# Kernel optimization log

Measured on AMD Instinct MI355X. Metric: run time of the kernel, lower is better.

Reference implementation:

```python
import jax, jax.numpy as jnp
import numpy as np

B, T, D, E, F, K = 1, 8192, 1024, 8, 4096, 2
CAP_FACTOR = 1.25
AUX_COEFF = 0.01


def setup_inputs() -> dict:
    key = jax.random.key(0)
    k0, k1, k2, k3, k4 = jax.random.split(key, 5)
    x = jax.random.normal(k0, (B, T, D), dtype=jnp.float32)
    Wr = jax.random.normal(k1, (E, D), dtype=jnp.float32) * 0.01  # router, std=0.01 per init
    s = 0.02
    Wg = jax.random.normal(k2, (E, F, D), dtype=jnp.float32) * s  # gate_proj per expert
    Wu = jax.random.normal(k3, (E, F, D), dtype=jnp.float32) * s  # up_proj per expert
    Wd = jax.random.normal(k4, (E, D, F), dtype=jnp.float32) * s  # down_proj per expert
    return {"x": x, "Wr": Wr, "Wg": Wg, "Wu": Wu, "Wd": Wd}


def reference(x, Wr, Wg, Wu, Wd):
    b, t, d = x.shape
    N = b * t
    capacity = max(int(t * K * CAP_FACTOR / E), 1)  # static, matches compute_capacity
    x_flat = x.reshape(N, d)

    # --- router ---
    logits = x_flat @ Wr.T                              # (N, E)
    probs = jax.nn.softmax(logits, axis=-1)
    topw_raw, topi = jax.lax.top_k(probs, K)            # (N, K)
    topw = topw_raw / (topw_raw.sum(-1, keepdims=True) + 1e-9)

    # --- dispatch order: slot-major (slot 0 over all tokens, then slot 1, ...) ---
    flat_e = topi.T.reshape(-1)                         # (K*N,) expert id per assignment
    flat_w = topw.T.reshape(-1)                         # (K*N,)
    tok = jnp.tile(jnp.arange(N), K)                    # (K*N,) token id per assignment

    oh = jax.nn.one_hot(flat_e, E, dtype=jnp.int32)     # (K*N, E)
    rank = (jnp.cumsum(oh, axis=0) - oh)[jnp.arange(K * N), flat_e]  # arrival rank per expert
    accepted = rank < capacity                          # dispatch_mask (slot-major flat)
    pos = jnp.where(accepted, rank, 0)
    dest = flat_e * capacity + pos                      # slot in flattened capacity buffer
    acc_f = accepted.astype(x.dtype)[:, None]

    # scatter tokens into capacity buffers (dropped tokens add zeros)
    buf = jnp.zeros((E * capacity, d), x.dtype).at[dest].add(x_flat[tok] * acc_f)
    expert_in = buf.reshape(E, capacity, d)

    # --- per-expert SwiGLU FFN (batched grouped GEMM) ---
    gate = jax.nn.silu(jnp.einsum('ecd,efd->ecf', expert_in, Wg))
    up = jnp.einsum('ecd,efd->ecf', expert_in, Wu)
    expert_out = jnp.einsum('ecf,edf->ecd', gate * up, Wd).reshape(E * capacity, d)

    # --- weighted combine back to token positions ---
    contrib = flat_w[:, None] * acc_f * expert_out[dest]
    out_flat = jnp.zeros((N, d), x.dtype).at[tok].add(contrib)
    output = out_flat.reshape(b, t, d)

    # --- load-balance aux loss ---
    counts = jnp.zeros(E, x.dtype).at[flat_e].add(accepted.astype(x.dtype))
    total = jnp.maximum(accepted.sum().astype(x.dtype), 1.0)
    f_i = counts / total
    P_i = probs.mean(0)
    aux_loss = AUX_COEFF * E * jnp.sum(f_i * P_i)
    return output, aux_loss
```

## Files before the change

kernel.cpp:

```cpp
#include <hip/hip_runtime.h>
#include <hip/hip_bf16.h>

#define N_TOK 8192
#define DIM   1024
#define NEXP  8
#define FF    4096
#define CAP   2560
#define NASSIGN (N_TOK * 2)
#define EOSL  ((size_t)NEXP * CAP * DIM)

typedef __bf16 bf16;
typedef __bf16 bf16x8 __attribute__((ext_vector_type(8)));
typedef __bf16 bf16x4v __attribute__((ext_vector_type(4)));
typedef float  f32x4  __attribute__((ext_vector_type(4)));

__device__ __forceinline__ void gl2lds16(const bf16* g, bf16* l) {
    __builtin_amdgcn_global_load_lds(
        (const __attribute__((address_space(1))) unsigned int*)g,
        (__attribute__((address_space(3))) unsigned int*)l,
        16, 0, 0);
}

template <int NT, int AST, int BST, int BG1, int BG2, class UnitFn, class EpiFn>
__device__ __forceinline__ void gemm256_persist(
    int nunits, UnitFn unit, EpiFn epi, int wave, int lane)
{
    __shared__ bf16 As[2 * 256 * 64];
    __shared__ bf16 Bs[2 * 256 * 64];

    const int wm = wave >> 2, wn = wave & 3;
    const int r16 = lane & 15, c16 = lane >> 4;
    const int wbase = wave * 8 * 64;

    auto STAGE = [&](const bf16* a, const bf16* bb, int buf) {
#pragma unroll
        for (int g = 0; g < 4; ++g)
            gl2lds16(a + (size_t)g * 64 * AST,
                     &As[buf * (256 * 64) + g * (64 * 64) + wbase]);
#pragma unroll
        for (int g = 0; g < 4; ++g)
            gl2lds16(bb + (size_t)((g & 1) * BG1 + (g >> 1) * BG2) * BST,
                     &Bs[buf * (256 * 64) + g * (64 * 64) + wbase]);
    };

    const bf16 *pA, *pB;
    unit(0, pA, pB);
    STAGE(pA, pB, 0);
    asm volatile("s_waitcnt vmcnt(0)" ::: "memory");
    __builtin_amdgcn_sched_barrier(0);
    __builtin_amdgcn_s_barrier();
    __builtin_amdgcn_sched_barrier(0);

    for (int u = 0; u < nunits; ++u) {
        const bf16 *pAn = pA, *pBn = pB;
        const bool more = (u + 1 < nunits);
        if (more) unit(u + 1, pAn, pBn);

        f32x4 acc[8][4] = {};
        for (int kt = 0; kt < NT; ++kt) {
            if (kt + 1 < NT)
                STAGE(pA + (size_t)(kt + 1) * 64, pB + (size_t)(kt + 1) * 64, (kt + 1) & 1);
            else if (more)
                STAGE(pAn, pBn, 0);

            const bf16* Asb = &As[(kt & 1) * (256 * 64)];
            const bf16* Bsb = &Bs[(kt & 1) * (256 * 64)];

            bf16x8 bfr[4][2];
#pragma unroll
            for (int nh = 0; nh < 2; ++nh)
#pragma unroll
                for (int np = 0; np < 2; ++np)
#pragma unroll
                    for (int kk = 0; kk < 2; ++kk) {
                        int rl = nh * 128 + wn * 32 + np * 16 + r16;
                        int phys = (kk * 4 + c16) ^ (rl & 7);
                        bfr[nh * 2 + np][kk] = *(const bf16x8*)&Bsb[rl * 64 + phys * 8];
                    }
#pragma unroll
            for (int mh = 0; mh < 2; ++mh) {
                bf16x8 af[4][2];
#pragma unroll
                for (int mm = 0; mm < 4; ++mm)
#pragma unroll
                    for (int kk = 0; kk < 2; ++kk) {
                        int row = wm * 128 + mh * 64 + mm * 16 + r16;
                        int phys = (kk * 4 + c16) ^ (row & 7);
                        af[mm][kk] = *(const bf16x8*)&Asb[row * 64 + phys * 8];
                    }
                __builtin_amdgcn_s_setprio(1);
#pragma unroll
                for (int mm = 0; mm < 4; ++mm)
#pragma unroll
                    for (int nf = 0; nf < 4; ++nf)
#pragma unroll
                        for (int kk = 0; kk < 2; ++kk)
                            acc[mh * 4 + mm][nf] =
                                __builtin_amdgcn_mfma_f32_16x16x32_bf16(
                                    af[mm][kk], bfr[nf][kk], acc[mh * 4 + mm][nf], 0, 0, 0);
                __builtin_amdgcn_s_setprio(0);
            }

            asm volatile("s_waitcnt vmcnt(0)" ::: "memory");
            __builtin_amdgcn_sched_barrier(0);
            __builtin_amdgcn_s_barrier();
            __builtin_amdgcn_sched_barrier(0);
        }
        epi(u, acc);
        pA = pAn; pB = pBn;
    }
}

__global__ __launch_bounds__(256) void cvt3_bf16_kernel(const float* __restrict__ a,
                                                        const float* __restrict__ b,
                                                        const float* __restrict__ c,
                                                        bf16* __restrict__ oa,
                                                        bf16* __restrict__ ob,
                                                        bf16* __restrict__ oc, int n) {
    const float* in = (blockIdx.y == 0) ? a : (blockIdx.y == 1) ? b : c;
    bf16*       out = (blockIdx.y == 0) ? oa : (blockIdx.y == 1) ? ob : oc;
    int stride = gridDim.x * blockDim.x * 8;
    for (int i = (blockIdx.x * blockDim.x + threadIdx.x) * 8; i < n; i += stride) {
        float4 x = *(const float4*)(in + i);
        float4 y = *(const float4*)(in + i + 4);
        bf16x8 o;
        o[0] = (bf16)x.x; o[1] = (bf16)x.y; o[2] = (bf16)x.z; o[3] = (bf16)x.w;
        o[4] = (bf16)y.x; o[5] = (bf16)y.y; o[6] = (bf16)y.z; o[7] = (bf16)y.w;
        *(bf16x8*)(out + i) = o;
    }
}

__global__ __launch_bounds__(256) void router_kernel(const float* __restrict__ x,
                                                     const float* __restrict__ Wr,
                                                     float* __restrict__ probs,
                                                     int* __restrict__ topi,
                                                     float* __restrict__ topw) {
    int wave = threadIdx.x >> 6;
    int lane = threadIdx.x & 63;
    int t = blockIdx.x * 4 + wave;
    const float* xr = x + (size_t)t * DIM;

    double acc[NEXP];
#pragma unroll
    for (int e = 0; e < NEXP; ++e) acc[e] = 0.0;
    for (int i = lane; i < DIM; i += 64) {
        double xv = (double)xr[i];
#pragma unroll
        for (int e = 0; e < NEXP; ++e) acc[e] += xv * (double)Wr[e * DIM + i];
    }
#pragma unroll
    for (int e = 0; e < NEXP; ++e) {
        double v = acc[e];
        for (int off = 32; off > 0; off >>= 1) v += __shfl_down(v, off, 64);
        acc[e] = v;
    }
    if (lane == 0) {
        double mx = acc[0];
        for (int e = 1; e < NEXP; ++e) if (acc[e] > mx) mx = acc[e];
        double p[NEXP], s = 0.0;
        for (int e = 0; e < NEXP; ++e) { p[e] = exp(acc[e] - mx); s += p[e]; }
        float pf[NEXP];
        for (int e = 0; e < NEXP; ++e) { pf[e] = (float)(p[e] / s); probs[t * NEXP + e] = pf[e]; }
        int e1 = 0;
        for (int e = 1; e < NEXP; ++e) if (acc[e] > acc[e1]) e1 = e;
        int e2 = -1;
        for (int e = 0; e < NEXP; ++e) {
            if (e == e1) continue;
            if (e2 < 0 || acc[e] > acc[e2]) e2 = e;
        }
        float w1 = pf[e1], w2 = pf[e2];
        float inv = 1.0f / (w1 + w2 + 1e-9f);
        topi[t * 2 + 0] = e1; topi[t * 2 + 1] = e2;
        topw[t * 2 + 0] = w1 * inv; topw[t * 2 + 1] = w2 * inv;
    }
}

__global__ __launch_bounds__(64) void rank_kernel(const int* __restrict__ topi,
                                                  int* __restrict__ dest,
                                                  int* __restrict__ accf,
                                                  int* __restrict__ counts) {
    int e = blockIdx.x;
    int lane = threadIdx.x;
    const int per = NASSIGN / 64;
    int base = lane * per;
    int cnt = 0;
    for (int i = 0; i < per; ++i) {
        int j = base + i;
        int t = j & (N_TOK - 1), s = j >> 13;
        if (topi[t * 2 + s] == e) cnt++;
    }
    int sum = cnt;
    for (int off = 1; off < 64; off <<= 1) {
        int v = __shfl_up(sum, off, 64);
        if (lane >= off) sum += v;
    }
    int r = sum - cnt;
    int total = __shfl(sum, 63, 64);
    for (int i = 0; i < per; ++i) {
        int j = base + i;
        int t = j & (N_TOK - 1), s = j >> 13;
        if (topi[t * 2 + s] == e) {
            int acc = (r < CAP) ? 1 : 0;
            dest[j] = e * CAP + (acc ? r : 0);
            accf[j] = acc;
            r++;
        }
    }
    if (lane == 63) counts[e] = (total < CAP) ? total : CAP;
}

__global__ __launch_bounds__(256) void gather_kernel(const float* __restrict__ x,
                                                     const int* __restrict__ dest,
                                                     const int* __restrict__ accf,
                                                     bf16* __restrict__ Xe) {
    int j = blockIdx.x;
    if (!accf[j]) return;
    int t = j & (N_TOK - 1);
    int d0 = threadIdx.x * 4;
    float4 v = *(const float4*)(x + (size_t)t * DIM + d0);
    union { bf16 h[4]; uint2 u; } tmp;
    tmp.h[0] = (bf16)v.x; tmp.h[1] = (bf16)v.y; tmp.h[2] = (bf16)v.z; tmp.h[3] = (bf16)v.w;
    *(uint2*)(Xe + (size_t)dest[j] * DIM + d0) = tmp.u;
}

__global__ __launch_bounds__(512, 2) void gateup_kernel(const bf16* __restrict__ Xe,
                                                        const bf16* __restrict__ Wg,
                                                        const bf16* __restrict__ Wu,
                                                        bf16* __restrict__ hbuf) {
    const int b = blockIdx.x;
    const int e = b & 7, r = b >> 3;
    const int tid = threadIdx.x, lane = tid & 63, wave = tid >> 6;
    const int wm = wave >> 2, wn = wave & 3;
    const int r16 = lane & 15, c16 = lane >> 4;

    const int l   = wave * 8 + (lane >> 3);
    const int csw = ((lane & 7) ^ (lane >> 3)) * 8;
    const int T = (l >> 4) & 1, wnl = l >> 5, r16l = l & 15;
    const bf16* XeE = Xe + (size_t)e * CAP * DIM + (size_t)l * DIM + csw;
    const bf16* WE  = (T ? Wu : Wg) + (size_t)e * FF * DIM
                    + (size_t)(wnl * 32 + r16l) * DIM + csw;
    bf16* hp = hbuf + (size_t)e * CAP * FF;

    auto unit = [&](int u, const bf16*& pA, const bf16*& pB) {
        int g = u * 32 + r;
        int m = g % 10, n = g / 10;
        pA = XeE + (size_t)(m * 256) * DIM;
        pB = WE + (size_t)(n * 128) * DIM;
    };
    auto epi = [&](int u, f32x4 (&acc)[8][4]) {
        int g = u * 32 + r;
        int m0 = (g % 10) * 256, n0f = (g / 10) * 128;
#pragma unroll
        for (int m = 0; m < 8; ++m)
#pragma unroll
            for (int cg = 0; cg < 2; ++cg)
#pragma unroll
                for (int j = 0; j < 4; ++j) {
                    float gg = acc[m][cg * 2 + 0][j];
                    float uu = acc[m][cg * 2 + 1][j];
                    float h = (gg / (1.f + __expf(-gg))) * uu;
                    int gr = m0 + wm * 128 + m * 16 + c16 * 4 + j;
                    int gc = n0f + wn * 32 + cg * 16 + r16;
                    hp[(size_t)gr * FF + gc] = (bf16)h;
                }
    };
    gemm256_persist<DIM / 64, DIM, DIM, 64, 16>(10, unit, epi, wave, lane);
}

__global__ __launch_bounds__(512, 2) void down_kernel(const bf16* __restrict__ hbuf,
                                                      const bf16* __restrict__ Wd,
                                                      bf16* __restrict__ eo) {
    const int b = blockIdx.x;
    const int e = b & 7, r = b >> 3;
    const int tid = threadIdx.x, lane = tid & 63, wave = tid >> 6;
    const int wm = wave >> 2, wn = wave & 3;
    const int r16 = lane & 15, c16 = lane >> 4;

    const int l   = wave * 8 + (lane >> 3);
    const int csw = ((lane & 7) ^ (lane >> 3)) * 8;
    const int nlow = (l >> 4) & 1, wnl = l >> 5, r16l = l & 15;
    const bf16* hb  = hbuf + (size_t)e * CAP * FF + (size_t)l * FF + csw;
    const bf16* WdE = Wd + (size_t)e * DIM * FF
                    + (size_t)(wnl * 64 + nlow * 16 + r16l) * FF + csw;
    bf16* eoE = eo + (size_t)e * CAP * DIM;

    auto unit = [&](int u, const bf16*& pA, const bf16*& pB) {
        int mk = u * 8 + (r & 7);
        int n  = r >> 3;
        int m = mk >> 2, kh = mk & 3;
        pA = hb + (size_t)(m * 256) * FF + kh * (FF / 4);
        pB = WdE + (size_t)(n * 256) * FF + kh * (FF / 4);
    };
    auto epi = [&](int u, f32x4 (&acc)[8][4]) {
        int mk = u * 8 + (r & 7);
        int m0 = (mk >> 2) * 256, kh = mk & 3;
        int n0 = (r >> 3) * 256;
        bf16* op = eoE + (size_t)kh * EOSL;
#pragma unroll
        for (int m = 0; m < 8; ++m)
#pragma unroll
            for (int nf = 0; nf < 4; ++nf)
#pragma unroll
                for (int j = 0; j < 4; ++j) {
                    int gr = m0 + wm * 128 + m * 16 + c16 * 4 + j;
                    int gc = n0 + wn * 64 + nf * 16 + r16;
                    op[(size_t)gr * DIM + gc] = (bf16)acc[m][nf][j];
                }
    };
    gemm256_persist<(FF / 4) / 64, FF, FF, 128, 32>(5, unit, epi, wave, lane);
}

__global__ __launch_bounds__(256) void combine_kernel(const bf16* __restrict__ eo,
                                                      const int* __restrict__ dest,
                                                      const int* __restrict__ accf,
                                                      const float* __restrict__ topw,
                                                      float* __restrict__ out) {
    int t = blockIdx.x;
    float w0 = accf[t] ? topw[t * 2 + 0] : 0.f;
    float w1 = accf[N_TOK + t] ? topw[t * 2 + 1] : 0.f;
    const bf16* a0 = eo + (size_t)dest[t] * DIM;
    const bf16* b0 = eo + (size_t)dest[N_TOK + t] * DIM;
    int d = threadIdx.x * 4;
    float ax = 0, ay = 0, az = 0, aw = 0, bx = 0, by = 0, bz = 0, bw = 0;
#pragma unroll
    for (int s4 = 0; s4 < 4; ++s4) {
        bf16x4v a = *(const bf16x4v*)(a0 + (size_t)s4 * EOSL + d);
        bf16x4v bb = *(const bf16x4v*)(b0 + (size_t)s4 * EOSL + d);
        ax += (float)a[0]; ay += (float)a[1]; az += (float)a[2]; aw += (float)a[3];
        bx += (float)bb[0]; by += (float)bb[1]; bz += (float)bb[2]; bw += (float)bb[3];
    }
    float4 o;
    o.x = w0 * ax + w1 * bx;
    o.y = w0 * ay + w1 * by;
    o.z = w0 * az + w1 * bz;
    o.w = w0 * aw + w1 * bw;
    *(float4*)(out + (size_t)t * DIM + d) = o;
}

__global__ __launch_bounds__(256) void aux_kernel(const float* __restrict__ probs,
                                                  const int* __restrict__ counts,
                                                  float* __restrict__ out_aux) {
    __shared__ float sm[256][NEXP];
    float loc[NEXP];
#pragma unroll
    for (int e = 0; e < NEXP; ++e) loc[e] = 0.f;
    for (int t = threadIdx.x; t < N_TOK; t += 256)
#pragma unroll
        for (int e = 0; e < NEXP; ++e) loc[e] += probs[t * NEXP + e];
#pragma unroll
    for (int e = 0; e < NEXP; ++e) sm[threadIdx.x][e] = loc[e];
    __syncthreads();
    for (int s = 128; s > 0; s >>= 1) {
        if (threadIdx.x < s)
#pragma unroll
            for (int e = 0; e < NEXP; ++e) sm[threadIdx.x][e] += sm[threadIdx.x + s][e];
        __syncthreads();
    }
    if (threadIdx.x == 0) {
        int tot = 0;
        for (int e = 0; e < NEXP; ++e) tot += counts[e];
        float totf = tot > 0 ? (float)tot : 1.f;
        float aux = 0.f;
        for (int e = 0; e < NEXP; ++e)
            aux += ((float)counts[e] / totf) * (sm[0][e] / (float)N_TOK);
        out_aux[0] = 0.01f * (float)NEXP * aux;
    }
}

extern "C" void kernel_launch(void* const* d_in, const int* in_sizes, int n_in,
                              void* d_out, int out_size, void* d_ws, size_t ws_size,
                              hipStream_t stream) {
    const float* x  = (const float*)d_in[0];
    const float* Wr = (const float*)d_in[1];
    const float* Wg = (const float*)d_in[2];
    const float* Wu = (const float*)d_in[3];
    const float* Wd = (const float*)d_in[4];
    float* out = (float*)d_out;

    char* ws = (char*)d_ws;
    size_t off = 0;
    auto alloc = [&](size_t bytes) -> void* {
        void* p = ws + off;
        off += (bytes + 255) & ~(size_t)255;
        return p;
    };
    const size_t NW = (size_t)NEXP * FF * DIM;
    bf16*  Wd_bf = (bf16*)alloc(NW * sizeof(bf16));
    bf16*  Wg_bf = (bf16*)alloc(NW * sizeof(bf16));
    bf16*  Wu_bf = (bf16*)alloc(NW * sizeof(bf16));
    bf16*  Xe    = (bf16*)alloc((size_t)NEXP * CAP * DIM * sizeof(bf16));
    bf16*  hbuf  = (bf16*)alloc((size_t)NEXP * CAP * FF * sizeof(bf16));
    float* probs = (float*)alloc((size_t)N_TOK * NEXP * sizeof(float));
    int*   topi  = (int*)alloc((size_t)N_TOK * 2 * sizeof(int));
    float* topw  = (float*)alloc((size_t)N_TOK * 2 * sizeof(float));
    int*   dst   = (int*)alloc((size_t)NASSIGN * sizeof(int));
    int*   accf  = (int*)alloc((size_t)NASSIGN * sizeof(int));
    int*   cnts  = (int*)alloc(NEXP * sizeof(int));
    bf16*  eo    = Wg_bf;

    cvt3_bf16_kernel<<<dim3(1024, 3), 256, 0, stream>>>(Wg, Wu, Wd, Wg_bf, Wu_bf, Wd_bf, (int)NW);
    router_kernel<<<N_TOK / 4, 256, 0, stream>>>(x, Wr, probs, topi, topw);
    rank_kernel<<<NEXP, 64, 0, stream>>>(topi, dst, accf, cnts);
    gather_kernel<<<NASSIGN, 256, 0, stream>>>(x, dst, accf, Xe);
    gateup_kernel<<<256, 512, 0, stream>>>(Xe, Wg_bf, Wu_bf, hbuf);
    down_kernel<<<256, 512, 0, stream>>>(hbuf, Wd_bf, eo);
    combine_kernel<<<N_TOK, 256, 0, stream>>>(eo, dst, accf, topw, out);
    aux_kernel<<<1, 256, 0, stream>>>(probs, cnts, out + (size_t)N_TOK * DIM);
}
```

Measured before the change: 830.2 us.

## Fuse gate/up and down GEMMs with per-expert flag barrier; merge prep kernels

The gate/up GEMM and the down GEMM become one persistent kernel. Each expert's 32 blocks sync through an atomic counter with a spin-wait, so an expert's down projection can start as soon as its own gate/up tiles finish, without waiting for a kernel boundary. The weight conversion and router kernels are merged into one launch. Buffers are regrouped into per-expert chunks (Wg, Wu, Xe) so expert outputs can overwrite that expert's consumed gate/up weights. The spin barrier adds a memset and assumes all blocks of an expert are co-resident on the device.

```diff
diff --git a/kernel.cpp b/kernel.cpp
--- a/kernel.cpp
+++ b/kernel.cpp
@@ -7,7 +7,9 @@
 #define FF    4096
 #define CAP   2560
 #define NASSIGN (N_TOK * 2)
-#define EOSL  ((size_t)NEXP * CAP * DIM)
+#define FFD   ((size_t)FF * DIM)
+#define CAPD  ((size_t)CAP * DIM)
+#define CH    (2 * FFD + CAPD)
 
 typedef __bf16 bf16;
 typedef __bf16 bf16x8 __attribute__((ext_vector_type(8)));
@@ -23,11 +25,8 @@
 
 template <int NT, int AST, int BST, int BG1, int BG2, class UnitFn, class EpiFn>
 __device__ __forceinline__ void gemm256_persist(
-    int nunits, UnitFn unit, EpiFn epi, int wave, int lane)
+    int nunits, UnitFn unit, EpiFn epi, int wave, int lane, bf16* As, bf16* Bs)
 {
-    __shared__ bf16 As[2 * 256 * 64];
-    __shared__ bf16 Bs[2 * 256 * 64];
-
     const int wm = wave >> 2, wn = wave & 3;
     const int r16 = lane & 15, c16 = lane >> 4;
     const int wbase = wave * 8 * 64;
@@ -111,33 +110,41 @@
     }
 }
 
-__global__ __launch_bounds__(256) void cvt3_bf16_kernel(const float* __restrict__ a,
-                                                        const float* __restrict__ b,
-                                                        const float* __restrict__ c,
-                                                        bf16* __restrict__ oa,
-                                                        bf16* __restrict__ ob,
-                                                        bf16* __restrict__ oc, int n) {
-    const float* in = (blockIdx.y == 0) ? a : (blockIdx.y == 1) ? b : c;
-    bf16*       out = (blockIdx.y == 0) ? oa : (blockIdx.y == 1) ? ob : oc;
-    int stride = gridDim.x * blockDim.x * 8;
-    for (int i = (blockIdx.x * blockDim.x + threadIdx.x) * 8; i < n; i += stride) {
-        float4 x = *(const float4*)(in + i);
-        float4 y = *(const float4*)(in + i + 4);
-        bf16x8 o;
-        o[0] = (bf16)x.x; o[1] = (bf16)x.y; o[2] = (bf16)x.z; o[3] = (bf16)x.w;
-        o[4] = (bf16)y.x; o[5] = (bf16)y.y; o[6] = (bf16)y.z; o[7] = (bf16)y.w;
-        *(bf16x8*)(out + i) = o;
-    }
-}
-
-__global__ __launch_bounds__(256) void router_kernel(const float* __restrict__ x,
-                                                     const float* __restrict__ Wr,
-                                                     float* __restrict__ probs,
-                                                     int* __restrict__ topi,
-                                                     float* __restrict__ topw) {
+__global__ __launch_bounds__(256) void prep_kernel(const float* __restrict__ Wg,
+                                                   const float* __restrict__ Wu,
+                                                   const float* __restrict__ Wd,
+                                                   bf16* __restrict__ chunks,
+                                                   bf16* __restrict__ Wd_bf,
+                                                   const float* __restrict__ x,
+                                                   const float* __restrict__ Wr,
+                                                   float* __restrict__ probs,
+                                                   int* __restrict__ topi,
+                                                   float* __restrict__ topw) {
+    if (blockIdx.x < 3072) {
+        const int which = blockIdx.x >> 10;
+        const int bx = blockIdx.x & 1023;
+        const float* in = (which == 0) ? Wg : (which == 1) ? Wu : Wd;
+        const int n = NEXP * (int)FFD;
+        const int stride = 1024 * 256 * 8;
+        for (int i = (bx * 256 + threadIdx.x) * 8; i < n; i += stride) {
+            float4 a = *(const float4*)(in + i);
+            float4 b = *(const float4*)(in + i + 4);
+            bf16x8 o;
+            o[0] = (bf16)a.x; o[1] = (bf16)a.y; o[2] = (bf16)a.z; o[3] = (bf16)a.w;
+            o[4] = (bf16)b.x; o[5] = (bf16)b.y; o[6] = (bf16)b.z; o[7] = (bf16)b.w;
+            if (which == 2) {
+                *(bf16x8*)(Wd_bf + i) = o;
+            } else {
+                int e = i >> 22;
+                size_t rem = (size_t)(i & ((1 << 22) - 1));
+                *(bf16x8*)(chunks + (size_t)e * CH + (which ? FFD : 0) + rem) = o;
+            }
+        }
+        return;
+    }
     int wave = threadIdx.x >> 6;
     int lane = threadIdx.x & 63;
-    int t = blockIdx.x * 4 + wave;
+    int t = (blockIdx.x - 3072) * 4 + wave;
     const float* xr = x + (size_t)t * DIM;
 
     double acc[NEXP];
@@ -212,21 +219,26 @@
 __global__ __launch_bounds__(256) void gather_kernel(const float* __restrict__ x,
                                                      const int* __restrict__ dest,
                                                      const int* __restrict__ accf,
-                                                     bf16* __restrict__ Xe) {
+                                                     bf16* __restrict__ chunks) {
     int j = blockIdx.x;
     if (!accf[j]) return;
     int t = j & (N_TOK - 1);
+    int d = dest[j];
+    int e = d / CAP, rr = d - e * CAP;
     int d0 = threadIdx.x * 4;
     float4 v = *(const float4*)(x + (size_t)t * DIM + d0);
     union { bf16 h[4]; uint2 u; } tmp;
     tmp.h[0] = (bf16)v.x; tmp.h[1] = (bf16)v.y; tmp.h[2] = (bf16)v.z; tmp.h[3] = (bf16)v.w;
-    *(uint2*)(Xe + (size_t)dest[j] * DIM + d0) = tmp.u;
-}
-
-__global__ __launch_bounds__(512, 2) void gateup_kernel(const bf16* __restrict__ Xe,
-                                                        const bf16* __restrict__ Wg,
-                                                        const bf16* __restrict__ Wu,
-                                                        bf16* __restrict__ hbuf) {
+    *(uint2*)(chunks + (size_t)e * CH + 2 * FFD + (size_t)rr * DIM + d0) = tmp.u;
+}
+
+__global__ __launch_bounds__(512, 2) void ffn_kernel(bf16* __restrict__ chunks,
+                                                     const bf16* __restrict__ Wd_bf,
+                                                     bf16* __restrict__ hbuf,
+                                                     int* __restrict__ flags) {
+    __shared__ bf16 As[2 * 256 * 64];
+    __shared__ bf16 Bs[2 * 256 * 64];
+
     const int b = blockIdx.x;
     const int e = b & 7, r = b >> 3;
     const int tid = threadIdx.x, lane = tid & 63, wave = tid >> 6;
@@ -235,82 +247,83 @@
 
     const int l   = wave * 8 + (lane >> 3);
     const int csw = ((lane & 7) ^ (lane >> 3)) * 8;
-    const int T = (l >> 4) & 1, wnl = l >> 5, r16l = l & 15;
-    const bf16* XeE = Xe + (size_t)e * CAP * DIM + (size_t)l * DIM + csw;
-    const bf16* WE  = (T ? Wu : Wg) + (size_t)e * FF * DIM
-                    + (size_t)(wnl * 32 + r16l) * DIM + csw;
-    bf16* hp = hbuf + (size_t)e * CAP * FF;
-
-    auto unit = [&](int u, const bf16*& pA, const bf16*& pB) {
-        int g = u * 32 + r;
-        int m = g % 10, n = g / 10;
-        pA = XeE + (size_t)(m * 256) * DIM;
-        pB = WE + (size_t)(n * 128) * DIM;
-    };
-    auto epi = [&](int u, f32x4 (&acc)[8][4]) {
-        int g = u * 32 + r;
-        int m0 = (g % 10) * 256, n0f = (g / 10) * 128;
-#pragma unroll
-        for (int m = 0; m < 8; ++m)
-#pragma unroll
-            for (int cg = 0; cg < 2; ++cg)
-#pragma unroll
-                for (int j = 0; j < 4; ++j) {
-                    float gg = acc[m][cg * 2 + 0][j];
-                    float uu = acc[m][cg * 2 + 1][j];
-                    float h = (gg / (1.f + __expf(-gg))) * uu;
-                    int gr = m0 + wm * 128 + m * 16 + c16 * 4 + j;
-                    int gc = n0f + wn * 32 + cg * 16 + r16;
-                    hp[(size_t)gr * FF + gc] = (bf16)h;
-                }
-    };
-    gemm256_persist<DIM / 64, DIM, DIM, 64, 16>(10, unit, epi, wave, lane);
-}
-
-__global__ __launch_bounds__(512, 2) void down_kernel(const bf16* __restrict__ hbuf,
-                                                      const bf16* __restrict__ Wd,
-                                                      bf16* __restrict__ eo) {
-    const int b = blockIdx.x;
-    const int e = b & 7, r = b >> 3;
-    const int tid = threadIdx.x, lane = tid & 63, wave = tid >> 6;
-    const int wm = wave >> 2, wn = wave & 3;
-    const int r16 = lane & 15, c16 = lane >> 4;
-
-    const int l   = wave * 8 + (lane >> 3);
-    const int csw = ((lane & 7) ^ (lane >> 3)) * 8;
-    const int nlow = (l >> 4) & 1, wnl = l >> 5, r16l = l & 15;
-    const bf16* hb  = hbuf + (size_t)e * CAP * FF + (size_t)l * FF + csw;
-    const bf16* WdE = Wd + (size_t)e * DIM * FF
-                    + (size_t)(wnl * 64 + nlow * 16 + r16l) * FF + csw;
-    bf16* eoE = eo + (size_t)e * CAP * DIM;
-
-    auto unit = [&](int u, const bf16*& pA, const bf16*& pB) {
-        int mk = u * 8 + (r & 7);
-        int n  = r >> 3;
-        int m = mk >> 2, kh = mk & 3;
-        pA = hb + (size_t)(m * 256) * FF + kh * (FF / 4);
-        pB = WdE + (size_t)(n * 256) * FF + kh * (FF / 4);
-    };
-    auto epi = [&](int u, f32x4 (&acc)[8][4]) {
-        int mk = u * 8 + (r & 7);
-        int m0 = (mk >> 2) * 256, kh = mk & 3;
-        int n0 = (r >> 3) * 256;
-        bf16* op = eoE + (size_t)kh * EOSL;
-#pragma unroll
-        for (int m = 0; m < 8; ++m)
-#pragma unroll
-            for (int nf = 0; nf < 4; ++nf)
-#pragma unroll
-                for (int j = 0; j < 4; ++j) {
-                    int gr = m0 + wm * 128 + m * 16 + c16 * 4 + j;
-                    int gc = n0 + wn * 64 + nf * 16 + r16;
-                    op[(size_t)gr * DIM + gc] = (bf16)acc[m][nf][j];
-                }
-    };
-    gemm256_persist<(FF / 4) / 64, FF, FF, 128, 32>(5, unit, epi, wave, lane);
-}
-
-__global__ __launch_bounds__(256) void combine_kernel(const bf16* __restrict__ eo,
+
+    {
+        const int T = (l >> 4) & 1, wnl = l >> 5, r16l = l & 15;
+        const bf16* XeE = chunks + (size_t)e * CH + 2 * FFD + (size_t)l * DIM + csw;
+        const bf16* WE  = chunks + (size_t)e * CH + (T ? FFD : 0)
+                        + (size_t)(wnl * 32 + r16l) * DIM + csw;
+        bf16* hp = hbuf + (size_t)e * CAP * FF;
+
+        auto unit = [&](int u, const bf16*& pA, const bf16*& pB) {
+            int g = u * 32 + r;
+            int m = g % 10, n = g / 10;
+            pA = XeE + (size_t)(m * 256) * DIM;
+            pB = WE + (size_t)(n * 128) * DIM;
+        };
+        auto epi = [&](int u, f32x4 (&acc)[8][4]) {
+            int g = u * 32 + r;
+            int m0 = (g % 10) * 256, n0f = (g / 10) * 128;
+#pragma unroll
+            for (int m = 0; m < 8; ++m)
+#pragma unroll
+                for (int cg = 0; cg < 2; ++cg)
+#pragma unroll
+                    for (int j = 0; j < 4; ++j) {
+                        float gg = acc[m][cg * 2 + 0][j];
+                        float uu = acc[m][cg * 2 + 1][j];
+                        float h = (gg / (1.f + __expf(-gg))) * uu;
+                        int gr = m0 + wm * 128 + m * 16 + c16 * 4 + j;
+                        int gc = n0f + wn * 32 + cg * 16 + r16;
+                        hp[(size_t)gr * FF + gc] = (bf16)h;
+                    }
+        };
+        gemm256_persist<DIM / 64, DIM, DIM, 64, 16>(10, unit, epi, wave, lane, As, Bs);
+    }
+
+    __syncthreads();
+    if (tid == 0) {
+        __hip_atomic_fetch_add(&flags[e], 1, __ATOMIC_RELEASE, __HIP_MEMORY_SCOPE_AGENT);
+        while (__hip_atomic_load(&flags[e], __ATOMIC_ACQUIRE, __HIP_MEMORY_SCOPE_AGENT) < 32) {}
+        __threadfence();
+    }
+    __syncthreads();
+
+    {
+        const int nlow = (l >> 4) & 1, wnl = l >> 5, r16l = l & 15;
+        const bf16* hb  = hbuf + (size_t)e * CAP * FF + (size_t)l * FF + csw;
+        const bf16* WdE = Wd_bf + (size_t)e * DIM * FF
+                        + (size_t)(wnl * 64 + nlow * 16 + r16l) * FF + csw;
+        bf16* eoE = chunks + (size_t)e * CH;
+
+        auto unit = [&](int u, const bf16*& pA, const bf16*& pB) {
+            int mk = u * 8 + (r & 7);
+            int n  = r >> 3;
+            int m = mk >> 2, kh = mk & 3;
+            pA = hb + (size_t)(m * 256) * FF + kh * (FF / 4);
+            pB = WdE + (size_t)(n * 256) * FF + kh * (FF / 4);
+        };
+        auto epi = [&](int u, f32x4 (&acc)[8][4]) {
+            int mk = u * 8 + (r & 7);
+            int m0 = (mk >> 2) * 256, kh = mk & 3;
+            int n0 = (r >> 3) * 256;
+            bf16* op = eoE + (size_t)kh * CAPD;
+#pragma unroll
+            for (int m = 0; m < 8; ++m)
+#pragma unroll
+                for (int nf = 0; nf < 4; ++nf)
+#pragma unroll
+                    for (int j = 0; j < 4; ++j) {
+                        int gr = m0 + wm * 128 + m * 16 + c16 * 4 + j;
+                        int gc = n0 + wn * 64 + nf * 16 + r16;
+                        op[(size_t)gr * DIM + gc] = (bf16)acc[m][nf][j];
+                    }
+        };
+        gemm256_persist<(FF / 4) / 64, FF, FF, 128, 32>(5, unit, epi, wave, lane, As, Bs);
+    }
+}
+
+__global__ __launch_bounds__(256) void combine_kernel(const bf16* __restrict__ chunks,
                                                       const int* __restrict__ dest,
                                                       const int* __restrict__ accf,
                                                       const float* __restrict__ topw,
@@ -318,14 +331,17 @@
     int t = blockIdx.x;
     float w0 = accf[t] ? topw[t * 2 + 0] : 0.f;
     float w1 = accf[N_TOK + t] ? topw[t * 2 + 1] : 0.f;
-    const bf16* a0 = eo + (size_t)dest[t] * DIM;
-    const bf16* b0 = eo + (size_t)dest[N_TOK + t] * DIM;
+    int d0a = dest[t], d0b = dest[N_TOK + t];
+    int ea = d0a / CAP, ra = d0a - ea * CAP;
+    int eb = d0b / CAP, rb = d0b - eb * CAP;
+    const bf16* a0 = chunks + (size_t)ea * CH + (size_t)ra * DIM;
+    const bf16* b0 = chunks + (size_t)eb * CH + (size_t)rb * DIM;
     int d = threadIdx.x * 4;
     float ax = 0, ay = 0, az = 0, aw = 0, bx = 0, by = 0, bz = 0, bw = 0;
 #pragma unroll
     for (int s4 = 0; s4 < 4; ++s4) {
-        bf16x4v a = *(const bf16x4v*)(a0 + (size_t)s4 * EOSL + d);
-        bf16x4v bb = *(const bf16x4v*)(b0 + (size_t)s4 * EOSL + d);
+        bf16x4v a = *(const bf16x4v*)(a0 + (size_t)s4 * CAPD + d);
+        bf16x4v bb = *(const bf16x4v*)(b0 + (size_t)s4 * CAPD + d);
         ax += (float)a[0]; ay += (float)a[1]; az += (float)a[2]; aw += (float)a[3];
         bx += (float)bb[0]; by += (float)bb[1]; bz += (float)bb[2]; bw += (float)bb[3];
     }
@@ -384,26 +400,23 @@
         off += (bytes + 255) & ~(size_t)255;
         return p;
     };
-    const size_t NW = (size_t)NEXP * FF * DIM;
-    bf16*  Wd_bf = (bf16*)alloc(NW * sizeof(bf16));
-    bf16*  Wg_bf = (bf16*)alloc(NW * sizeof(bf16));
-    bf16*  Wu_bf = (bf16*)alloc(NW * sizeof(bf16));
-    bf16*  Xe    = (bf16*)alloc((size_t)NEXP * CAP * DIM * sizeof(bf16));
-    bf16*  hbuf  = (bf16*)alloc((size_t)NEXP * CAP * FF * sizeof(bf16));
-    float* probs = (float*)alloc((size_t)N_TOK * NEXP * sizeof(float));
-    int*   topi  = (int*)alloc((size_t)N_TOK * 2 * sizeof(int));
-    float* topw  = (float*)alloc((size_t)N_TOK * 2 * sizeof(float));
-    int*   dst   = (int*)alloc((size_t)NASSIGN * sizeof(int));
-    int*   accf  = (int*)alloc((size_t)NASSIGN * sizeof(int));
-    int*   cnts  = (int*)alloc(NEXP * sizeof(int));
-    bf16*  eo    = Wg_bf;
-
-    cvt3_bf16_kernel<<<dim3(1024, 3), 256, 0, stream>>>(Wg, Wu, Wd, Wg_bf, Wu_bf, Wd_bf, (int)NW);
-    router_kernel<<<N_TOK / 4, 256, 0, stream>>>(x, Wr, probs, topi, topw);
+    const size_t NW = (size_t)NEXP * FFD;
+    bf16*  chunks = (bf16*)alloc((size_t)NEXP * CH * sizeof(bf16));
+    bf16*  Wd_bf  = (bf16*)alloc(NW * sizeof(bf16));
+    bf16*  hbuf   = (bf16*)alloc((size_t)NEXP * CAP * FF * sizeof(bf16));
+    float* probs  = (float*)alloc((size_t)N_TOK * NEXP * sizeof(float));
+    int*   topi   = (int*)alloc((size_t)N_TOK * 2 * sizeof(int));
+    float* topw   = (float*)alloc((size_t)N_TOK * 2 * sizeof(float));
+    int*   dst    = (int*)alloc((size_t)NASSIGN * sizeof(int));
+    int*   accf   = (int*)alloc((size_t)NASSIGN * sizeof(int));
+    int*   cnts   = (int*)alloc(NEXP * sizeof(int));
+    int*   flags  = (int*)alloc(NEXP * sizeof(int));
+
+    hipMemsetAsync(flags, 0, NEXP * sizeof(int), stream);
+    prep_kernel<<<5120, 256, 0, stream>>>(Wg, Wu, Wd, chunks, Wd_bf, x, Wr, probs, topi, topw);
     rank_kernel<<<NEXP, 64, 0, stream>>>(topi, dst, accf, cnts);
-    gather_kernel<<<NASSIGN, 256, 0, stream>>>(x, dst, accf, Xe);
-    gateup_kernel<<<256, 512, 0, stream>>>(Xe, Wg_bf, Wu_bf, hbuf);
-    down_kernel<<<256, 512, 0, stream>>>(hbuf, Wd_bf, eo);
-    combine_kernel<<<N_TOK, 256, 0, stream>>>(eo, dst, accf, topw, out);
+    gather_kernel<<<NASSIGN, 256, 0, stream>>>(x, dst, accf, chunks);
+    ffn_kernel<<<256, 512, 0, stream>>>(chunks, Wd_bf, hbuf, flags);
+    combine_kernel<<<N_TOK, 256, 0, stream>>>(chunks, dst, accf, topw, out);
     aux_kernel<<<1, 256, 0, stream>>>(probs, cnts, out + (size_t)N_TOK * DIM);
 }
```

Result: slower. 878.9 us (+5.9%).
